# Performance work log

Measured on AMD Instinct MI355X. Metric: run time of the kernel, lower is better.

Reference implementation:

```python
import jax, jax.numpy as jnp
import numpy as np

B = 2048          # number of trees (batch)
K = 511           # nodes per complete binary tree (depth 9: levels 0..8)
DEPTH = 9
VOCAB = 200000
EDIM = 128


def setup_inputs() -> dict:
    key = jax.random.key(0)
    k1, k2, k3, k4 = jax.random.split(key, 4)
    N = B * K
    i = np.arange(K)
    lvl = np.floor(np.log2(i + 1)).astype(np.int32)            # level within tree, 0..8
    par_local = np.where(i > 0, (i - 1) // 2, 0).astype(np.int64)  # root points to itself
    offs = (np.arange(B, dtype=np.int64) * K)[:, None]
    parent = jnp.asarray((offs + par_local[None, :]).reshape(-1), dtype=jnp.int32)
    level = jnp.asarray(np.tile(lvl, B), dtype=jnp.int32)
    batch_id = jnp.asarray(np.repeat(np.arange(B, dtype=np.int64), K), dtype=jnp.int32)
    tokens = jax.random.randint(k1, (N,), 0, VOCAB, dtype=jnp.int32)
    emb_weight = jax.random.normal(k2, (VOCAB, EDIM), dtype=jnp.float32) * 0.02
    W = jax.random.normal(k3, (EDIM, EDIM), dtype=jnp.float32) * 0.05
    b = jax.random.normal(k4, (EDIM,), dtype=jnp.float32) * 0.01
    return {"emb_weight": emb_weight, "W": W, "b": b,
            "tokens": tokens, "parent": parent, "level": level, "batch_id": batch_id}


def reference(emb_weight, W, b, tokens, parent, level, batch_id):
    # per-node projection: W_c(embedding(token))  -> [N, EDIM]
    h = emb_weight[tokens] @ W + b
    # bottom-up child aggregation: h[parent] += h[child], deepest level first
    for l in range(DEPTH - 1, 0, -1):
        contrib = jnp.where((level == l)[:, None], h, 0.0)
        h = h.at[parent].add(contrib)
    # torch.max over all node_list snapshots == per-tree elementwise max of node
    # states, clamped at 0 by the zero rows of untouched batch_node snapshots.
    seg_max = jax.ops.segment_max(h, batch_id, num_segments=B)
    return jnp.maximum(seg_max, 0.0)
```

## Files before the change

### kernel.cpp

```cpp
#include <hip/hip_runtime.h>
#include <hip/hip_bf16.h>
#include <stdint.h>

#define VOCAB 200000
#define EDIM 128
#define NTREES 2048
#define KNODES 511

typedef __attribute__((ext_vector_type(4))) float f32x4;
typedef __attribute__((ext_vector_type(2))) float f32x2;
typedef __attribute__((ext_vector_type(8))) short s16x8;
typedef __attribute__((ext_vector_type(8))) unsigned short u16x8;
typedef __attribute__((ext_vector_type(4))) unsigned int u32x4;

#define AS1 __attribute__((address_space(1)))
#define AS3 __attribute__((address_space(3)))

__device__ __forceinline__ unsigned short f2bf(float x) {
  unsigned u = __builtin_bit_cast(unsigned, x);
  return (unsigned short)((u + 0x7fffu + ((u >> 16) & 1u)) >> 16);
}
__device__ __forceinline__ float bf2f(unsigned short h) {
  unsigned u = ((unsigned)h) << 16;
  return __builtin_bit_cast(float, u);
}

__device__ __forceinline__ unsigned fp8enc(float v) {
  unsigned u = __builtin_bit_cast(unsigned, v);
  unsigned s = (u >> 24) & 0x80u;
  unsigned au = u & 0x7fffffffu;
  au = au > 0x43E00000u ? 0x43E00000u : au;
  unsigned r = au + 0x0007ffffu + ((au >> 20) & 1u);
  unsigned code = (((r >> 23) - 120u) << 3) | ((r >> 20) & 7u);
  float a = __builtin_bit_cast(float, au);
  unsigned sub = (unsigned)(int)rintf(a * 512.0f);
  unsigned c = (au < 0x3C800000u) ? sub : code;
  return c | s;
}
__device__ __forceinline__ float fp8dec(unsigned b) {
  unsigned e = (b >> 3) & 15u, m = b & 7u;
  float n = __builtin_bit_cast(float, ((e + 120u) << 23) | (m << 20));
  float sv = (float)(int)m * 0.001953125f;
  float v = e ? n : sv;
  return (b & 0x80u) ? -v : v;
}

__device__ __forceinline__ unsigned enc4(float a, float b, float c, float d) {
#if __has_builtin(__builtin_amdgcn_cvt_pk_fp8_f32)
  int pk = 0;
  pk = __builtin_amdgcn_cvt_pk_fp8_f32(a, b, pk, false);
  pk = __builtin_amdgcn_cvt_pk_fp8_f32(c, d, pk, true);
  return (unsigned)pk;
#else
  return fp8enc(a) | (fp8enc(b) << 8) | (fp8enc(c) << 16) | (fp8enc(d) << 24);
#endif
}

__device__ __forceinline__ void dec8(uint2 v, float* o) {
#if __has_builtin(__builtin_amdgcn_cvt_pk_f32_fp8)
  f32x2 a = __builtin_amdgcn_cvt_pk_f32_fp8(v.x, false);
  f32x2 b = __builtin_amdgcn_cvt_pk_f32_fp8(v.x, true);
  f32x2 c = __builtin_amdgcn_cvt_pk_f32_fp8(v.y, false);
  f32x2 d = __builtin_amdgcn_cvt_pk_f32_fp8(v.y, true);
  o[0] = a[0]; o[1] = a[1]; o[2] = b[0]; o[3] = b[1];
  o[4] = c[0]; o[5] = c[1]; o[6] = d[0]; o[7] = d[1];
#else
#pragma unroll
  for (int i = 0; i < 4; ++i) o[i] = fp8dec((v.x >> (8 * i)) & 0xFFu);
#pragma unroll
  for (int i = 0; i < 4; ++i) o[4 + i] = fp8dec((v.y >> (8 * i)) & 0xFFu);
#endif
}

__device__ __forceinline__ s16x8 cvt8(f32x4 a, f32x4 b) {
  u16x8 t;
#pragma unroll
  for (int i = 0; i < 4; ++i)
    t[i] = __builtin_bit_cast(unsigned short, __float2bfloat16(a[i]));
#pragma unroll
  for (int i = 0; i < 4; ++i)
    t[4 + i] = __builtin_bit_cast(unsigned short, __float2bfloat16(b[i]));
  return __builtin_bit_cast(s16x8, t);
}

__global__ __launch_bounds__(256) void wprep_kernel(
    const float* __restrict__ W, const float* __restrict__ b,
    unsigned short* __restrict__ WTb2, float* __restrict__ bsc) {
  int c = blockIdx.x * 256 + threadIdx.x;
  if (c < 2048) {
    int lane = c & 63, fr = c >> 6;
    int ks = fr >> 3, nt = fr & 7, q = lane >> 4, cl = lane & 15;
    u16x8 t;
#pragma unroll
    for (int j = 0; j < 8; ++j)
      t[j] = f2bf(W[(ks * 32 + q * 8 + j) * EDIM + nt * 16 + cl] * 64.0f);
    *(u16x8*)(WTb2 + c * 8) = t;
  }
  if (c < EDIM) bsc[c] = b[c] * 64.0f;
}

__global__ __launch_bounds__(256, 3) void proj_kernel(
    const float* __restrict__ emb, const unsigned short* __restrict__ WTb2,
    const float* __restrict__ bsc, unsigned char* __restrict__ T8) {
  __shared__ unsigned short WL[2048 * 8];
  __shared__ float LB[EDIM];
  __shared__ char ST[4][32 * 144];

  const int tid = threadIdx.x;
  const int wv = tid >> 6, lane = tid & 63;
  const int q = lane >> 4, cl = lane & 15;

  const long rowbase = (long)blockIdx.x * 128 + wv * 32;
  long r0 = rowbase + cl, r1 = rowbase + 16 + cl;
  if (r0 >= VOCAB) r0 = VOCAB - 1;
  if (r1 >= VOCAB) r1 = VOCAB - 1;
  const float* p0 = emb + r0 * EDIM + q * 8;
  const float* p1 = emb + r1 * EDIM + q * 8;
  f32x4 ea0[4], eb0[4], ea1[4], eb1[4];
#pragma unroll
  for (int ks = 0; ks < 4; ++ks) {
    ea0[ks] = *(const f32x4*)(p0 + ks * 32);
    eb0[ks] = *(const f32x4*)(p0 + ks * 32 + 4);
    ea1[ks] = *(const f32x4*)(p1 + ks * 32);
    eb1[ks] = *(const f32x4*)(p1 + ks * 32 + 4);
  }

#pragma unroll
  for (int i = 0; i < 8; ++i) {
    const char* src = (const char*)WTb2 + wv * 8192 + i * 1024 + lane * 16;
    char* dstp = (char*)WL + wv * 8192 + i * 1024;
    __builtin_amdgcn_global_load_lds((const AS1 unsigned int*)src,
                                     (AS3 unsigned int*)dstp, 16, 0, 0);
  }
  if (tid < EDIM) LB[tid] = bsc[tid];

  __syncthreads();

  f32x4 acc[2][8];
#pragma unroll
  for (int nt = 0; nt < 8; ++nt) {
    f32x4 bv = *(const f32x4*)(LB + nt * 16 + q * 4);
    acc[0][nt] = bv;
    acc[1][nt] = bv;
  }
#pragma unroll
  for (int ks = 0; ks < 4; ++ks) {
    s16x8 ef0 = cvt8(ea0[ks], eb0[ks]);
    s16x8 ef1 = cvt8(ea1[ks], eb1[ks]);
#pragma unroll
    for (int nt = 0; nt < 8; ++nt) {
      s16x8 wf = *(const s16x8*)((const char*)WL + (ks * 8 + nt) * 1024 + lane * 16);
      acc[0][nt] = __builtin_amdgcn_mfma_f32_16x16x32_bf16(wf, ef0, acc[0][nt], 0, 0, 0);
      acc[1][nt] = __builtin_amdgcn_mfma_f32_16x16x32_bf16(wf, ef1, acc[1][nt], 0, 0, 0);
    }
  }

  char* sw = &ST[wv][0];
#pragma unroll
  for (int rt = 0; rt < 2; ++rt)
#pragma unroll
    for (int nt = 0; nt < 8; ++nt) {
      unsigned pk = enc4(acc[rt][nt][0], acc[rt][nt][1], acc[rt][nt][2], acc[rt][nt][3]);
      *(unsigned*)(sw + (rt * 16 + cl) * 144 + (nt * 4 + q) * 4) = pk;
    }
  asm volatile("s_waitcnt lgkmcnt(0)" ::: "memory");
  __builtin_amdgcn_sched_barrier(0);

#pragma unroll
  for (int j = 0; j < 4; ++j) {
    const int slot = j * 64 + lane;
    const int rr = slot >> 3, c16 = slot & 7;
    const long grow = rowbase + rr;
    if (grow < VOCAB) {
      u32x4 v = *(const u32x4*)(sw + rr * 144 + c16 * 16);
      *(u32x4*)&T8[grow * EDIM + c16 * 16] = v;
    }
  }
}

__global__ __launch_bounds__(512, 4) void tree_kernel(
    const unsigned char* __restrict__ T8, const int* __restrict__ tokens,
    float* __restrict__ out) {
  __shared__ unsigned char P8[512][EDIM];
  unsigned char* lds = &P8[0][0];
  const int SOFF = 16384;
  const int MOFF = 53248;

  const int tid = threadIdx.x;
  const int tree = blockIdx.x;
  const int wv = tid >> 6, lane = tid & 63;

  const int* tk = tokens + (long)tree * KNODES;
  int toks[8];
#pragma unroll
  for (int i = 0; i < 8; ++i) {
    int node = wv * 64 + i * 8 + (lane >> 3);
    toks[i] = tk[node > 510 ? 510 : node];
  }
  const int chunk = (lane & 7) ^ ((lane >> 3) & 7);
#pragma unroll
  for (int i = 0; i < 8; ++i) {
    const unsigned char* src = T8 + (long)toks[i] * EDIM + chunk * 16;
    unsigned char* dst = &P8[wv * 64 + i * 8][0];
    __builtin_amdgcn_global_load_lds((const AS1 unsigned int*)src,
                                     (AS3 unsigned int*)dst, 16, 0, 0);
  }
  __syncthreads();

  auto ldP8 = [&](int row, int q8) -> uint2 {
    int g = q8 >> 1, h = q8 & 1;
    return *(const uint2*)(lds + row * 128 + (((g ^ (row & 7))) << 4) + h * 8);
  };
  auto saddr = [&](int slot, int q16) -> unsigned char* {
    return lds + SOFF + slot * 288 + ((q16 ^ (slot & 7)) << 4);
  };

  const int q = tid & 15;
  const int jg = tid >> 4;
  float rmax[8];
#pragma unroll
  for (int e = 0; e < 8; ++e) rmax[e] = 0.f;

  u16x8 sp7[4];
#pragma unroll
  for (int k = 0; k < 4; ++k) {
    const int p = jg + 32 * k, m = 127 + p;
    uint2 pr = ldP8(m, q);
    uint2 xr = ldP8(2 * m + 1, q);
    uint2 yr = ldP8(2 * m + 2, q);
    float pv[8], xv[8], yv[8];
    dec8(pr, pv); dec8(xr, xv); dec8(yr, yv);
#pragma unroll
    for (int e = 0; e < 8; ++e) {
      float sv = pv[e] + xv[e] + yv[e];
      rmax[e] = fmaxf(rmax[e], fmaxf(fmaxf(xv[e], yv[e]), sv));
      sp7[k][e] = f2bf(sv);
    }
  }
  __syncthreads();
#pragma unroll
  for (int k = 0; k < 4; ++k) *(u16x8*)saddr(jg + 32 * k, q) = sp7[k];
  __syncthreads();

  for (int l = 6; l >= 0; --l) {
    const int cnt = 1 << l;
    for (int p = jg; p < cnt; p += 32) {
      const int m = cnt - 1 + p;
      const int ps = p << (7 - l);
      const int c2s = ps + (1 << (6 - l));
      uint2 pr = ldP8(m, q);
      u16x8 c1 = *(const u16x8*)saddr(ps, q);
      u16x8 c2 = *(const u16x8*)saddr(c2s, q);
      float pv[8];
      dec8(pr, pv);
      u16x8 sp;
#pragma unroll
      for (int e = 0; e < 8; ++e) {
        float sv = pv[e] + bf2f(c1[e]) + bf2f(c2[e]);
        rmax[e] = fmaxf(rmax[e], sv);
        sp[e] = f2bf(sv);
      }
      *(u16x8*)saddr(ps, q) = sp;
    }
    __syncthreads();
  }

#pragma unroll
  for (int e = 0; e < 8; ++e) {
    rmax[e] = fmaxf(rmax[e], __shfl_xor(rmax[e], 16, 64));
    rmax[e] = fmaxf(rmax[e], __shfl_xor(rmax[e], 32, 64));
  }
  float* mb = (float*)(lds + MOFF);
  if (lane < 16) {
#pragma unroll
    for (int e = 0; e < 8; ++e) mb[wv * 128 + lane * 8 + e] = rmax[e];
  }
  __syncthreads();
  if (tid < 128) {
    float v = mb[tid];
#pragma unroll
    for (int w2 = 1; w2 < 8; ++w2) v = fmaxf(v, mb[w2 * 128 + tid]);
    out[(long)tree * 128 + tid] = v * 0.015625f;
  }
}

extern "C" void kernel_launch(void* const* d_in, const int* in_sizes, int n_in,
                              void* d_out, int out_size, void* d_ws, size_t ws_size,
                              hipStream_t stream) {
  const float* emb = (const float*)d_in[0];
  const float* W = (const float*)d_in[1];
  const float* b = (const float*)d_in[2];
  const int* tokens = (const int*)d_in[3];

  unsigned char* T8 = (unsigned char*)d_ws;
  unsigned short* WTb2 = (unsigned short*)((char*)d_ws + (32 << 20));
  float* bsc = (float*)((char*)d_ws + (32 << 20) + 32768);
  float* out = (float*)d_out;

  wprep_kernel<<<8, 256, 0, stream>>>(W, b, WTb2, bsc);
  proj_kernel<<<1563, 256, 0, stream>>>(emb, WTb2, bsc, T8);
  tree_kernel<<<NTREES, 512, 0, stream>>>(T8, tokens, out);
}
```

Before: 64.55 us.

## Halve rows per wave in projection, reuse weight LDS for staging

The projection kernel now has each wave handle 16 vocabulary rows instead of 32, so blocks cover 64 rows and the grid doubles to VOCAB/64. The separate staging shared buffer is removed; after a second barrier the packed 8-bit outputs are staged in the weight LDS region. Lower register and LDS use allows a higher occupancy bound (4 blocks per SM). The cost is twice as many blocks, each reloading the full weight matrix into LDS, and one extra barrier. Bounds checks are dropped because VOCAB divides evenly by 64.

```diff
diff --git a/kernel.cpp b/kernel.cpp
--- a/kernel.cpp
+++ b/kernel.cpp
@@ -99,30 +99,23 @@
   if (c < EDIM) bsc[c] = b[c] * 64.0f;
 }
 
-__global__ __launch_bounds__(256, 3) void proj_kernel(
+__global__ __launch_bounds__(256, 4) void proj_kernel(
     const float* __restrict__ emb, const unsigned short* __restrict__ WTb2,
     const float* __restrict__ bsc, unsigned char* __restrict__ T8) {
   __shared__ unsigned short WL[2048 * 8];
   __shared__ float LB[EDIM];
-  __shared__ char ST[4][32 * 144];
 
   const int tid = threadIdx.x;
   const int wv = tid >> 6, lane = tid & 63;
   const int q = lane >> 4, cl = lane & 15;
 
-  const long rowbase = (long)blockIdx.x * 128 + wv * 32;
-  long r0 = rowbase + cl, r1 = rowbase + 16 + cl;
-  if (r0 >= VOCAB) r0 = VOCAB - 1;
-  if (r1 >= VOCAB) r1 = VOCAB - 1;
-  const float* p0 = emb + r0 * EDIM + q * 8;
-  const float* p1 = emb + r1 * EDIM + q * 8;
-  f32x4 ea0[4], eb0[4], ea1[4], eb1[4];
+  const long rowbase = (long)blockIdx.x * 64 + wv * 16;
+  const float* p0 = emb + (rowbase + cl) * EDIM + q * 8;
+  f32x4 ea[4], eb[4];
 #pragma unroll
   for (int ks = 0; ks < 4; ++ks) {
-    ea0[ks] = *(const f32x4*)(p0 + ks * 32);
-    eb0[ks] = *(const f32x4*)(p0 + ks * 32 + 4);
-    ea1[ks] = *(const f32x4*)(p1 + ks * 32);
-    eb1[ks] = *(const f32x4*)(p1 + ks * 32 + 4);
+    ea[ks] = *(const f32x4*)(p0 + ks * 32);
+    eb[ks] = *(const f32x4*)(p0 + ks * 32 + 4);
   }
 
 #pragma unroll
@@ -134,47 +127,44 @@
   }
   if (tid < EDIM) LB[tid] = bsc[tid];
 
-  __syncthreads();
-
-  f32x4 acc[2][8];
-#pragma unroll
-  for (int nt = 0; nt < 8; ++nt) {
-    f32x4 bv = *(const f32x4*)(LB + nt * 16 + q * 4);
-    acc[0][nt] = bv;
-    acc[1][nt] = bv;
-  }
 #pragma unroll
   for (int ks = 0; ks < 4; ++ks) {
-    s16x8 ef0 = cvt8(ea0[ks], eb0[ks]);
-    s16x8 ef1 = cvt8(ea1[ks], eb1[ks]);
+    asm volatile("" : "+v"(ea[ks]));
+    asm volatile("" : "+v"(eb[ks]));
+  }
+  __syncthreads();
+
+  f32x4 acc[8];
+#pragma unroll
+  for (int nt = 0; nt < 8; ++nt) acc[nt] = *(const f32x4*)(LB + nt * 16 + q * 4);
+#pragma unroll
+  for (int ks = 0; ks < 4; ++ks) {
+    s16x8 ef = cvt8(ea[ks], eb[ks]);
 #pragma unroll
     for (int nt = 0; nt < 8; ++nt) {
       s16x8 wf = *(const s16x8*)((const char*)WL + (ks * 8 + nt) * 1024 + lane * 16);
-      acc[0][nt] = __builtin_amdgcn_mfma_f32_16x16x32_bf16(wf, ef0, acc[0][nt], 0, 0, 0);
-      acc[1][nt] = __builtin_amdgcn_mfma_f32_16x16x32_bf16(wf, ef1, acc[1][nt], 0, 0, 0);
+      acc[nt] = __builtin_amdgcn_mfma_f32_16x16x32_bf16(wf, ef, acc[nt], 0, 0, 0);
     }
   }
 
-  char* sw = &ST[wv][0];
-#pragma unroll
-  for (int rt = 0; rt < 2; ++rt)
-#pragma unroll
-    for (int nt = 0; nt < 8; ++nt) {
-      unsigned pk = enc4(acc[rt][nt][0], acc[rt][nt][1], acc[rt][nt][2], acc[rt][nt][3]);
-      *(unsigned*)(sw + (rt * 16 + cl) * 144 + (nt * 4 + q) * 4) = pk;
-    }
+  __syncthreads();
+
+  char* sw = (char*)WL + wv * 8192 + cl * 144;
+#pragma unroll
+  for (int nt = 0; nt < 8; ++nt) {
+    unsigned pk = enc4(acc[nt][0], acc[nt][1], acc[nt][2], acc[nt][3]);
+    *(unsigned*)(sw + (nt * 4 + q) * 4) = pk;
+  }
   asm volatile("s_waitcnt lgkmcnt(0)" ::: "memory");
   __builtin_amdgcn_sched_barrier(0);
 
-#pragma unroll
-  for (int j = 0; j < 4; ++j) {
+  const long tb8 = rowbase * EDIM;
+#pragma unroll
+  for (int j = 0; j < 2; ++j) {
     const int slot = j * 64 + lane;
     const int rr = slot >> 3, c16 = slot & 7;
-    const long grow = rowbase + rr;
-    if (grow < VOCAB) {
-      u32x4 v = *(const u32x4*)(sw + rr * 144 + c16 * 16);
-      *(u32x4*)&T8[grow * EDIM + c16 * 16] = v;
-    }
+    u32x4 v = *(const u32x4*)((char*)WL + wv * 8192 + rr * 144 + c16 * 16);
+    *(u32x4*)&T8[tb8 + slot * 16] = v;
   }
 }
 
@@ -298,6 +288,6 @@
   float* out = (float*)d_out;
 
   wprep_kernel<<<8, 256, 0, stream>>>(W, b, WTb2, bsc);
-  proj_kernel<<<1563, 256, 0, stream>>>(emb, WTb2, bsc, T8);
+  proj_kernel<<<VOCAB / 64, 256, 0, stream>>>(emb, WTb2, bsc, T8);
   tree_kernel<<<NTREES, 512, 0, stream>>>(T8, tokens, out);
 }
```

Result: faster. 63.12 us (-2.2%).
